# Optimization experiments

Hardware: AMD Instinct MI355X
Metric: run time of the kernel (lower is better)

Reference implementation:

```python
import math
import jax, jax.numpy as jnp
import numpy as np

D_MODEL = 1024
HEADS = 16
D_K = D_MODEL // HEADS
BATCH = 4
SEQ = 2048


def setup_inputs() -> dict:
    key = jax.random.key(0)
    ks = jax.random.split(key, 7)
    q = jax.random.normal(ks[0], (BATCH, SEQ, D_MODEL), dtype=jnp.float32)
    k = jax.random.normal(ks[1], (BATCH, SEQ, D_MODEL), dtype=jnp.float32)
    v = jax.random.normal(ks[2], (BATCH, SEQ, D_MODEL), dtype=jnp.float32)
    # causal mask: True = masked (filled with -inf), broadcastable over batch & heads
    mask = jnp.triu(jnp.ones((SEQ, SEQ), dtype=bool), k=1)[None, None, :, :]
    s = 1.0 / math.sqrt(D_MODEL)
    Wq = jax.random.normal(ks[3], (D_MODEL, D_MODEL), dtype=jnp.float32) * s
    Wk = jax.random.normal(ks[4], (D_MODEL, D_MODEL), dtype=jnp.float32) * s
    Wv = jax.random.normal(ks[5], (D_MODEL, D_MODEL), dtype=jnp.float32) * s
    Wo = jax.random.normal(ks[6], (D_MODEL, D_MODEL), dtype=jnp.float32) * s
    return {"q": q, "k": k, "v": v, "mask": mask, "Wq": Wq, "Wk": Wk, "Wv": Wv, "Wo": Wo}


def reference(q, k, v, mask, Wq, Wk, Wv, Wo):
    B, S, _ = q.shape
    # Linear(d_model, d_model, bias=False): y = x @ W.T
    def proj(x, W):
        return (x @ W.T).reshape(B, S, HEADS, D_K).transpose(0, 2, 1, 3)  # [B,H,S,Dk]
    qh, kh, vh = proj(q, Wq), proj(k, Wk), proj(v, Wv)
    scores = jnp.einsum('bhqd,bhkd->bhqk', qh, kh) / math.sqrt(D_K)
    scores = jnp.where(mask, -jnp.inf, scores)
    attn = jax.nn.softmax(scores, axis=-1)  # dropout p=0 is identity
    ctx = jnp.einsum('bhqk,bhkd->bhqd', attn, vh)
    ctx = ctx.transpose(0, 2, 1, 3).reshape(B, S, D_MODEL)
    return ctx @ Wo.T
```

## Files before the change

kernel.cpp:

```cpp
#include <hip/hip_runtime.h>
#include <hip/hip_bf16.h>
#include <stdint.h>

#define S_LEN 2048
#define DMODEL 1024
#define HEADS 16
#define DK 64
#define LDK 72

#define QSCALE 0.18033688011112042f

typedef __attribute__((ext_vector_type(8))) short bf16x8;
typedef __attribute__((ext_vector_type(4))) float f32x4;

__device__ __forceinline__ unsigned short f2bf(float f) {
    union { float f; unsigned u; } c; c.f = f;
    unsigned u = c.u;
    u += 0x7fffu + ((u >> 16) & 1u);
    return (unsigned short)(u >> 16);
}

__device__ __forceinline__ unsigned pkbf(float a, float b) {
    union { float f; unsigned u; } ca, cb; ca.f = a; cb.f = b;
    unsigned ua = ca.u + (0x7fffu + ((ca.u >> 16) & 1u));
    unsigned ub = cb.u + (0x7fffu + ((cb.u >> 16) & 1u));
    return __builtin_amdgcn_perm(ub, ua, 0x07060302);
}

__device__ __forceinline__ unsigned cvtpk(float a, float b) {
    unsigned r;
    asm("v_cvt_pk_bf16_f32 %0, %1, %2" : "=v"(r) : "v"(a), "v"(b));
    return r;
}

__device__ __forceinline__ void g2lds16(const unsigned short* g, unsigned short* l) {
    __builtin_amdgcn_global_load_lds((const __attribute__((address_space(1))) void*)g,
                                     (__attribute__((address_space(3))) void*)l, 16, 0, 0);
}

__global__ __launch_bounds__(256) void convert_kernel(
    const float* __restrict__ q, const float* __restrict__ k, const float* __restrict__ v,
    const float* __restrict__ Wq, const float* __restrict__ Wk, const float* __restrict__ Wv,
    const float* __restrict__ Wo,
    unsigned short* __restrict__ qbf, unsigned short* __restrict__ kbf,
    unsigned short* __restrict__ vbf, unsigned short* __restrict__ wbf)
{
    const float* src; unsigned short* dst; int n8;
    const int y = blockIdx.y;
    if (y == 0)      { src = q;  dst = qbf;           n8 = 1048576; }
    else if (y == 1) { src = k;  dst = kbf;           n8 = 1048576; }
    else if (y == 2) { src = v;  dst = vbf;           n8 = 1048576; }
    else if (y == 3) { src = Wq; dst = wbf;           n8 = 131072; }
    else if (y == 4) { src = Wk; dst = wbf + 1048576; n8 = 131072; }
    else if (y == 5) { src = Wv; dst = wbf + 2097152; n8 = 131072; }
    else             { src = Wo; dst = wbf + 3145728; n8 = 131072; }
    int i = blockIdx.x * 256 + threadIdx.x;
    if (i >= n8) return;
    float4 f0 = ((const float4*)src)[(size_t)2 * i];
    float4 f1 = ((const float4*)src)[(size_t)2 * i + 1];
    union { unsigned u[4]; uint4 v; } o;
    o.u[0] = pkbf(f0.x, f0.y); o.u[1] = pkbf(f0.z, f0.w);
    o.u[2] = pkbf(f1.x, f1.y); o.u[3] = pkbf(f1.z, f1.w);
    *(uint4*)&dst[(size_t)8 * i] = o.v;
}

__device__ __forceinline__ void gemm_core_256x128(
    const unsigned short* __restrict__ Apanel,
    const unsigned short* __restrict__ Bpanel,
    unsigned short* sm,
    f32x4 acc[4][4])
{
    const int t    = threadIdx.x;
    const int lane = t & 63;
    const int w    = t >> 6;
    const int wm   = w >> 1;
    const int wn   = w & 1;
    const int lrow = lane & 15;
    const int quad = lane >> 4;

    const int l8   = lane >> 3;
    const int c16s = (lane & 7) ^ l8;
    const unsigned short* gA = Apanel + (size_t)(w * 8 + l8) * 1024 + c16s * 8;
    const unsigned short* gB = Bpanel + (size_t)(w * 8 + l8) * 1024 + c16s * 8;
    unsigned short* lA = sm + w * 512;
    unsigned short* lB = sm + 16384 + w * 512;

#define STAGE_KT(bufsel, kt) do {                                         \
        unsigned short* la = lA + (bufsel) * 24576;                       \
        unsigned short* lb = lB + (bufsel) * 24576;                       \
        const unsigned short* ga = gA + (kt) * 64;                        \
        const unsigned short* gb = gB + (kt) * 64;                        \
        g2lds16(ga,                        la);                           \
        g2lds16(ga + (size_t) 64 * 1024,   la + 4096);                    \
        g2lds16(ga + (size_t)128 * 1024,   la + 8192);                    \
        g2lds16(ga + (size_t)192 * 1024,   la + 12288);                   \
        g2lds16(gb,                        lb);                           \
        g2lds16(gb + (size_t) 64 * 1024,   lb + 4096);                    \
    } while (0)

    for (int i = 0; i < 4; i++) for (int j = 0; j < 4; j++) acc[i][j] = (f32x4){0.f, 0.f, 0.f, 0.f};

    STAGE_KT(0, 0);

#pragma unroll 1
    for (int kt = 0; kt < 16; ++kt) {
        const int buf = kt & 1;
        if (kt < 15) {
            STAGE_KT(buf ^ 1, kt + 1);
            asm volatile("s_waitcnt vmcnt(6)" ::: "memory");
        } else {
            asm volatile("s_waitcnt vmcnt(0)" ::: "memory");
        }
        __builtin_amdgcn_sched_barrier(0);
        __builtin_amdgcn_s_barrier();
        __builtin_amdgcn_sched_barrier(0);

        const unsigned short* tA = sm + buf * 24576;
        const unsigned short* tB = sm + buf * 24576 + 16384;
        for (int kh = 0; kh < 2; ++kh) {
            const int cs = ((kh * 4 + quad) ^ (lrow & 7)) * 8;
            bf16x8 a[4], b[4];
            for (int mi = 0; mi < 4; mi++)
                a[mi] = *(const bf16x8*)&tA[(wm * 64 + mi * 16 + lrow) * 64 + cs];
            for (int nj = 0; nj < 4; nj++)
                b[nj] = *(const bf16x8*)&tB[(wn * 64 + nj * 16 + lrow) * 64 + cs];
            __builtin_amdgcn_s_setprio(1);
            for (int mi = 0; mi < 4; mi++)
                for (int nj = 0; nj < 4; nj++)
                    acc[mi][nj] = __builtin_amdgcn_mfma_f32_16x16x32_bf16(a[mi], b[nj], acc[mi][nj], 0, 0, 0);
            __builtin_amdgcn_s_setprio(0);
        }
        __builtin_amdgcn_sched_barrier(0);
        __builtin_amdgcn_s_barrier();
        __builtin_amdgcn_sched_barrier(0);
    }
#undef STAGE_KT
}

__global__ __launch_bounds__(512, 2) void proj_gemm_kernel(
    const unsigned short* __restrict__ qbf, const unsigned short* __restrict__ kbf,
    const unsigned short* __restrict__ vbf, const unsigned short* __restrict__ wbf,
    unsigned short* __restrict__ qh, unsigned short* __restrict__ kh,
    unsigned short* __restrict__ vh_t)
{
    const unsigned short* A; const unsigned short* Bm; unsigned short* Y;
    const int z = blockIdx.z;
    if (z == 0)      { A = qbf; Bm = wbf;           Y = qh;   }
    else if (z == 1) { A = kbf; Bm = wbf + 1048576; Y = kh;   }
    else             { A = vbf; Bm = wbf + 2097152; Y = vh_t; }

    __shared__ unsigned short sm[49152];

    const int m0 = blockIdx.x * 256;
    const int n0 = blockIdx.y * 128;

    f32x4 acc[4][4];
    gemm_core_256x128(A + (size_t)m0 * 1024, Bm + (size_t)n0 * 1024, sm, acc);

    const int t = threadIdx.x, lane = t & 63;
    const int wm = (t >> 6) >> 1, wn = (t >> 6) & 1;
    const int lrow = lane & 15, quad = lane >> 4;
    const float scale = (z == 0) ? QSCALE : 1.0f;
    for (int i = 0; i < 4; i++) {
        int grow = m0 + wm * 64 + i * 16 + quad * 4;
        for (int j = 0; j < 4; j++) {
            int gcol = n0 + wn * 64 + j * 16 + lrow;
            int h = gcol >> 6, d = gcol & 63;
            for (int r = 0; r < 4; r++) {
                int row = grow + r;
                int b_ = row >> 11;
                int s_ = row & 2047;
                unsigned short val = f2bf(acc[i][j][r] * scale);
                if (z == 2)
                    Y[(((size_t)(b_ * HEADS + h) * DK) + d) * S_LEN + s_] = val;
                else
                    Y[(((size_t)(b_ * HEADS + h) * S_LEN) + s_) * DK + d] = val;
            }
        }
    }
}

__global__ __launch_bounds__(512, 2) void outproj_gemm_kernel(
    const unsigned short* __restrict__ ctx, const unsigned short* __restrict__ wobf,
    float* __restrict__ out)
{
    __shared__ unsigned short sm[49152];

    const int m0 = blockIdx.x * 256;
    const int n0 = blockIdx.y * 128;

    f32x4 acc[4][4];
    gemm_core_256x128(ctx + (size_t)m0 * 1024, wobf + (size_t)n0 * 1024, sm, acc);

    const int t = threadIdx.x, lane = t & 63;
    const int wm = (t >> 6) >> 1, wn = (t >> 6) & 1;
    const int lrow = lane & 15, quad = lane >> 4;
    for (int i = 0; i < 4; i++) {
        int grow = m0 + wm * 64 + i * 16 + quad * 4;
        for (int j = 0; j < 4; j++) {
            int gcol = n0 + wn * 64 + j * 16 + lrow;
            for (int r = 0; r < 4; r++)
                out[(size_t)(grow + r) * DMODEL + gcol] = acc[i][j][r];
        }
    }
}

__global__ __launch_bounds__(256) void attn_kernel(
    const unsigned short* __restrict__ qh, const unsigned short* __restrict__ kh,
    const unsigned short* __restrict__ vh_t, unsigned short* __restrict__ ctx)
{
    __shared__ unsigned short sK[64 * LDK];
    __shared__ unsigned short sVt[64 * LDK];
    __shared__ unsigned short sPT[4][32 * LDK];

    const int t    = threadIdx.x;
    const int lane = t & 63;
    const int wid  = t >> 6;
    const int lin  = (int)(blockIdx.y * gridDim.x + blockIdx.x);
    const int wlin = (lin & 7) * 64 + (lin >> 3);
    const int qx   = wlin & 7;
    const int bh   = wlin >> 3;
    const size_t base = (size_t)bh * S_LEN * DK;
    const int lrow = lane & 15;
    const int quad = lane >> 4;
    const int b_ = bh >> 4, h_ = bh & 15;
    unsigned short* myPT = &sPT[wid][0];

    const int sr0 = t >> 3;
    const int sc0 = (t & 7) * 8;
    const unsigned short* gK = kh + base;
    const unsigned short* gV = vh_t + base;

    for (int pass = 0; pass < 2; ++pass) {
        const int qt = pass ? (15 - qx) : qx;
        const int q0 = qt * 128;
        const int qw0 = q0 + wid * 32;

        bf16x8 qreg[2][2];
        for (int nf = 0; nf < 2; ++nf)
            for (int h = 0; h < 2; ++h)
                qreg[nf][h] = *(const bf16x8*)&qh[base + (size_t)(qw0 + nf * 16 + lrow) * DK + h * 32 + quad * 8];

        f32x4 o[4][2];
        for (int mf = 0; mf < 4; mf++) for (int nf = 0; nf < 2; nf++) o[mf][nf] = (f32x4){0.f, 0.f, 0.f, 0.f};
        float lstat[2] = { 0.f, 0.f };

        const int ntiles = q0 / 64 + 2;

        uint4 rK0 = *(const uint4*)&gK[(size_t)sr0 * DK + sc0];
        uint4 rK1 = *(const uint4*)&gK[(size_t)(sr0 + 32) * DK + sc0];
        uint4 rV0 = *(const uint4*)&gV[(size_t)sr0 * S_LEN + sc0];
        uint4 rV1 = *(const uint4*)&gV[(size_t)(sr0 + 32) * S_LEN + sc0];

        for (int kt = 0; kt < ntiles; ++kt) {
            const int k0 = kt * 64;
            __syncthreads();
            *(uint4*)&sK [sr0 * LDK + sc0]        = rK0;
            *(uint4*)&sK [(sr0 + 32) * LDK + sc0] = rK1;
            *(uint4*)&sVt[sr0 * LDK + sc0]        = rV0;
            *(uint4*)&sVt[(sr0 + 32) * LDK + sc0] = rV1;
            if (kt + 1 < ntiles) {
                const int kn = k0 + 64;
                rK0 = *(const uint4*)&gK[(size_t)(kn + sr0) * DK + sc0];
                rK1 = *(const uint4*)&gK[(size_t)(kn + sr0 + 32) * DK + sc0];
                rV0 = *(const uint4*)&gV[(size_t)sr0 * S_LEN + kn + sc0];
                rV1 = *(const uint4*)&gV[(size_t)(sr0 + 32) * S_LEN + kn + sc0];
            }
            __syncthreads();

            if (k0 > qw0 + 31) continue;

            f32x4 st[4][2];
            for (int mf = 0; mf < 4; mf++) for (int nf = 0; nf < 2; nf++) st[mf][nf] = (f32x4){0.f, 0.f, 0.f, 0.f};
            for (int h = 0; h < 2; ++h) {
                bf16x8 kf[4];
                for (int mf = 0; mf < 4; mf++)
                    kf[mf] = *(const bf16x8*)&sK[(mf * 16 + lrow) * LDK + h * 32 + quad * 8];
                __builtin_amdgcn_s_setprio(1);
                for (int mf = 0; mf < 4; mf++)
                    for (int nf = 0; nf < 2; nf++)
                        st[mf][nf] = __builtin_amdgcn_mfma_f32_16x16x32_bf16(kf[mf], qreg[nf][h], st[mf][nf], 0, 0, 0);
                __builtin_amdgcn_s_setprio(0);
            }

            const bool need_mask = (k0 + 63 > qw0);

            for (int nf = 0; nf < 2; ++nf) {
                const int qidx = qw0 + nf * 16 + lrow;
                if (need_mask) {
                    for (int mf = 0; mf < 4; mf++)
                        for (int r = 0; r < 4; r++) {
                            int key = k0 + mf * 16 + quad * 4 + r;
                            if (key > qidx) st[mf][nf][r] = -INFINITY;
                        }
                }
                float rsum = 0.f;
                for (int mf = 0; mf < 4; mf++) {
                    float p0 = exp2f(st[mf][nf][0]);
                    float p1 = exp2f(st[mf][nf][1]);
                    float p2 = exp2f(st[mf][nf][2]);
                    float p3 = exp2f(st[mf][nf][3]);
                    rsum += (p0 + p1) + (p2 + p3);
                    uint2 pk;
                    pk.x = cvtpk(p0, p1);
                    pk.y = cvtpk(p2, p3);
                    *(uint2*)&myPT[(nf * 16 + lrow) * LDK + mf * 16 + quad * 4] = pk;
                }
                lstat[nf] += rsum;
            }

            for (int h = 0; h < 2; ++h) {
                bf16x8 vf[4], pf[2];
                for (int mf = 0; mf < 4; mf++)
                    vf[mf] = *(const bf16x8*)&sVt[(mf * 16 + lrow) * LDK + h * 32 + quad * 8];
                for (int nf = 0; nf < 2; nf++)
                    pf[nf] = *(const bf16x8*)&myPT[(nf * 16 + lrow) * LDK + h * 32 + quad * 8];
                __builtin_amdgcn_s_setprio(1);
                for (int mf = 0; mf < 4; mf++)
                    for (int nf = 0; nf < 2; nf++)
                        o[mf][nf] = __builtin_amdgcn_mfma_f32_16x16x32_bf16(vf[mf], pf[nf], o[mf][nf], 0, 0, 0);
                __builtin_amdgcn_s_setprio(0);
            }
        }

        for (int nf = 0; nf < 2; ++nf) {
            float ls = lstat[nf];
            ls += __shfl_xor(ls, 16);
            ls += __shfl_xor(ls, 32);
            float inv = 1.f / ls;
            int s_ = qw0 + nf * 16 + lrow;
            size_t rowbase = (((size_t)(b_ * S_LEN + s_)) * HEADS + h_) * DK;
            for (int mf = 0; mf < 4; mf++) {
                int d0 = mf * 16 + quad * 4;
                uint2 pk;
                pk.x = pkbf(o[mf][nf][0] * inv, o[mf][nf][1] * inv);
                pk.y = pkbf(o[mf][nf][2] * inv, o[mf][nf][3] * inv);
                *(uint2*)&ctx[rowbase + d0] = pk;
            }
        }
    }
}

__global__ __launch_bounds__(256) void proj_fb_kernel(
    const float* __restrict__ q, const float* __restrict__ k, const float* __restrict__ v,
    const float* __restrict__ Wq, const float* __restrict__ Wk, const float* __restrict__ Wv,
    unsigned short* __restrict__ qh, unsigned short* __restrict__ kh, unsigned short* __restrict__ vh_t)
{
    const float* X; const float* W; unsigned short* Y;
    if (blockIdx.z == 0)      { X = q; W = Wq; Y = qh; }
    else if (blockIdx.z == 1) { X = k; W = Wk; Y = kh; }
    else                      { X = v; W = Wv; Y = vh_t; }

    __shared__ short sA[128 * LDK];
    __shared__ short sB[128 * LDK];
    const int t = threadIdx.x, lane = t & 63, wid = t >> 6;
    const int wrow = (wid >> 1) * 64, wcol = (wid & 1) * 64;
    const int m0 = blockIdx.x * 128, n0 = blockIdx.y * 128;
    const int lrow = lane & 15, quad = lane >> 4, lk = quad * 8;

    f32x4 acc[4][4];
    for (int i = 0; i < 4; i++) for (int j = 0; j < 4; j++) acc[i][j] = (f32x4){0.f, 0.f, 0.f, 0.f};

    for (int kb = 0; kb < DMODEL; kb += 64) {
        for (int it = 0; it < 8; ++it) {
            int idx = t + it * 256;
            int row = idx >> 4, c4 = (idx & 15) * 4;
            float4 fa = *(const float4*)&X[(size_t)(m0 + row) * DMODEL + kb + c4];
            float4 fb = *(const float4*)&W[(size_t)(n0 + row) * DMODEL + kb + c4];
            short4 sa = { (short)f2bf(fa.x), (short)f2bf(fa.y), (short)f2bf(fa.z), (short)f2bf(fa.w) };
            short4 sb = { (short)f2bf(fb.x), (short)f2bf(fb.y), (short)f2bf(fb.z), (short)f2bf(fb.w) };
            *(short4*)&sA[row * LDK + c4] = sa;
            *(short4*)&sB[row * LDK + c4] = sb;
        }
        __syncthreads();
        for (int kk = 0; kk < 64; kk += 32) {
            bf16x8 a[4], b[4];
            for (int i = 0; i < 4; i++) a[i] = *(const bf16x8*)&sA[(wrow + i * 16 + lrow) * LDK + kk + lk];
            for (int j = 0; j < 4; j++) b[j] = *(const bf16x8*)&sB[(wcol + j * 16 + lrow) * LDK + kk + lk];
            for (int i = 0; i < 4; i++)
                for (int j = 0; j < 4; j++)
                    acc[i][j] = __builtin_amdgcn_mfma_f32_16x16x32_bf16(a[i], b[j], acc[i][j], 0, 0, 0);
        }
        __syncthreads();
    }

    const float scale = (blockIdx.z == 0) ? QSCALE : 1.0f;
    for (int i = 0; i < 4; i++) {
        int grow = m0 + wrow + i * 16 + quad * 4;
        for (int j = 0; j < 4; j++) {
            int gcol = n0 + wcol + j * 16 + lrow;
            int h = gcol >> 6, d = gcol & 63;
            for (int r = 0; r < 4; r++) {
                int row = grow + r, b_ = row >> 11, s_ = row & 2047;
                unsigned short val = f2bf(acc[i][j][r] * scale);
                if (blockIdx.z == 2)
                    Y[(((size_t)(b_ * HEADS + h) * DK) + d) * S_LEN + s_] = val;
                else
                    Y[(((size_t)(b_ * HEADS + h) * S_LEN) + s_) * DK + d] = val;
            }
        }
    }
}

__global__ __launch_bounds__(256) void outproj_fb_kernel(
    const unsigned short* __restrict__ ctx, const float* __restrict__ Wo, float* __restrict__ out)
{
    __shared__ short sA[128 * LDK];
    __shared__ short sB[128 * LDK];
    const int t = threadIdx.x, lane = t & 63, wid = t >> 6;
    const int wrow = (wid >> 1) * 64, wcol = (wid & 1) * 64;
    const int m0 = blockIdx.x * 128, n0 = blockIdx.y * 128;
    const int lrow = lane & 15, quad = lane >> 4, lk = quad * 8;

    f32x4 acc[4][4];
    for (int i = 0; i < 4; i++) for (int j = 0; j < 4; j++) acc[i][j] = (f32x4){0.f, 0.f, 0.f, 0.f};

    for (int kb = 0; kb < DMODEL; kb += 64) {
        for (int it = 0; it < 4; ++it) {
            int idx = t + it * 256;
            int row = idx >> 3, c8 = (idx & 7) * 8;
            *(uint4*)&sA[row * LDK + c8] = *(const uint4*)&ctx[(size_t)(m0 + row) * DMODEL + kb + c8];
        }
        for (int it = 0; it < 8; ++it) {
            int idx = t + it * 256;
            int row = idx >> 4, c4 = (idx & 15) * 4;
            float4 fb = *(const float4*)&Wo[(size_t)(n0 + row) * DMODEL + kb + c4];
            short4 sb = { (short)f2bf(fb.x), (short)f2bf(fb.y), (short)f2bf(fb.z), (short)f2bf(fb.w) };
            *(short4*)&sB[row * LDK + c4] = sb;
        }
        __syncthreads();
        for (int kk = 0; kk < 64; kk += 32) {
            bf16x8 a[4], b[4];
            for (int i = 0; i < 4; i++) a[i] = *(const bf16x8*)&sA[(wrow + i * 16 + lrow) * LDK + kk + lk];
            for (int j = 0; j < 4; j++) b[j] = *(const bf16x8*)&sB[(wcol + j * 16 + lrow) * LDK + kk + lk];
            for (int i = 0; i < 4; i++)
                for (int j = 0; j < 4; j++)
                    acc[i][j] = __builtin_amdgcn_mfma_f32_16x16x32_bf16(a[i], b[j], acc[i][j], 0, 0, 0);
        }
        __syncthreads();
    }

    for (int i = 0; i < 4; i++) {
        int grow = m0 + wrow + i * 16 + quad * 4;
        for (int j = 0; j < 4; j++) {
            int gcol = n0 + wcol + j * 16 + lrow;
            for (int r = 0; r < 4; r++)
                out[(size_t)(grow + r) * DMODEL + gcol] = acc[i][j][r];
        }
    }
}

extern "C" void kernel_launch(void* const* d_in, const int* in_sizes, int n_in,
                              void* d_out, int out_size, void* d_ws, size_t ws_size,
                              hipStream_t stream)
{
    const float* q  = (const float*)d_in[0];
    const float* k  = (const float*)d_in[1];
    const float* v  = (const float*)d_in[2];
    const float* Wq = (const float*)d_in[4];
    const float* Wk = (const float*)d_in[5];
    const float* Wv = (const float*)d_in[6];
    const float* Wo = (const float*)d_in[7];
    float* out = (float*)d_out;

    const size_t M8 = (size_t)8 * 1024 * 1024;
    const size_t need = (size_t)(52) * 1024 * 1024 * 2;

    if (ws_size >= need) {
        unsigned short* qbf  = (unsigned short*)d_ws;
        unsigned short* kbf  = qbf + M8;
        unsigned short* vbf  = kbf + M8;
        unsigned short* wbf  = vbf + M8;
        unsigned short* qh   = wbf + (size_t)4 * 1024 * 1024;
        unsigned short* kh   = qh + M8;
        unsigned short* vh_t = kh + M8;
        unsigned short* ctx  = qbf;

        dim3 gCvt(4096, 7);
        convert_kernel<<<gCvt, 256, 0, stream>>>(q, k, v, Wq, Wk, Wv, Wo, qbf, kbf, vbf, wbf);

        dim3 gProj(32, 8, 3);
        proj_gemm_kernel<<<gProj, 512, 0, stream>>>(qbf, kbf, vbf, wbf, qh, kh, vh_t);

        dim3 gAttn(8, 64);
        attn_kernel<<<gAttn, 256, 0, stream>>>(qh, kh, vh_t, ctx);

        dim3 gOut(32, 8);
        outproj_gemm_kernel<<<gOut, 512, 0, stream>>>(ctx, wbf + (size_t)3 * 1024 * 1024, out);
    } else {
        unsigned short* qh   = (unsigned short*)d_ws;
        unsigned short* kh   = qh + M8;
        unsigned short* vh_t = kh + M8;
        unsigned short* ctx  = vh_t + M8;

        dim3 gProj(64, 8, 3);
        proj_fb_kernel<<<gProj, 256, 0, stream>>>(q, k, v, Wq, Wk, Wv, qh, kh, vh_t);

        dim3 gAttn(8, 64);
        attn_kernel<<<gAttn, 256, 0, stream>>>(qh, kh, vh_t, ctx);

        dim3 gOut(64, 8);
        outproj_fb_kernel<<<gOut, 256, 0, stream>>>(ctx, Wo, out);
    }
}
```

Before: 326.8 us.

## Halve attention query tile to 64 rows and double block count

Attention blocks now handle a 64-row query tile per pass (16 rows per wave) instead of 128, with the grid doubled to 16x64 blocks and the causal mask applied only on the diagonal tile. Launch bounds request 4 blocks per CU and the per-wave P scratch is halved. This raises parallelism and occupancy and removes per-wave skipped tiles. In exchange, every K/V tile is loaded into shared memory twice as often per query row, and each wave issues fewer MFMAs per load.

```diff
diff --git a/kernel.cpp b/kernel.cpp
--- a/kernel.cpp
+++ b/kernel.cpp
@@ -205,21 +205,21 @@
     }
 }
 
-__global__ __launch_bounds__(256) void attn_kernel(
+__global__ __launch_bounds__(256, 4) void attn_kernel(
     const unsigned short* __restrict__ qh, const unsigned short* __restrict__ kh,
     const unsigned short* __restrict__ vh_t, unsigned short* __restrict__ ctx)
 {
     __shared__ unsigned short sK[64 * LDK];
     __shared__ unsigned short sVt[64 * LDK];
-    __shared__ unsigned short sPT[4][32 * LDK];
+    __shared__ unsigned short sPT[4][16 * LDK];
 
     const int t    = threadIdx.x;
     const int lane = t & 63;
     const int wid  = t >> 6;
     const int lin  = (int)(blockIdx.y * gridDim.x + blockIdx.x);
-    const int wlin = (lin & 7) * 64 + (lin >> 3);
-    const int qx   = wlin & 7;
-    const int bh   = wlin >> 3;
+    const int wlin = (lin & 7) * 128 + (lin >> 3);
+    const int qx   = wlin & 15;
+    const int bh   = wlin >> 4;
     const size_t base = (size_t)bh * S_LEN * DK;
     const int lrow = lane & 15;
     const int quad = lane >> 4;
@@ -232,20 +232,19 @@
     const unsigned short* gV = vh_t + base;
 
     for (int pass = 0; pass < 2; ++pass) {
-        const int qt = pass ? (15 - qx) : qx;
-        const int q0 = qt * 128;
-        const int qw0 = q0 + wid * 32;
-
-        bf16x8 qreg[2][2];
-        for (int nf = 0; nf < 2; ++nf)
-            for (int h = 0; h < 2; ++h)
-                qreg[nf][h] = *(const bf16x8*)&qh[base + (size_t)(qw0 + nf * 16 + lrow) * DK + h * 32 + quad * 8];
-
-        f32x4 o[4][2];
-        for (int mf = 0; mf < 4; mf++) for (int nf = 0; nf < 2; nf++) o[mf][nf] = (f32x4){0.f, 0.f, 0.f, 0.f};
-        float lstat[2] = { 0.f, 0.f };
-
-        const int ntiles = q0 / 64 + 2;
+        const int qt = pass ? (31 - qx) : qx;
+        const int q0 = qt * 64;
+        const int qw0 = q0 + wid * 16;
+
+        bf16x8 qreg[2];
+        for (int h = 0; h < 2; ++h)
+            qreg[h] = *(const bf16x8*)&qh[base + (size_t)(qw0 + lrow) * DK + h * 32 + quad * 8];
+
+        f32x4 o[4];
+        for (int mf = 0; mf < 4; mf++) o[mf] = (f32x4){0.f, 0.f, 0.f, 0.f};
+        float lstat = 0.f;
+
+        const int ntiles = qt + 1;
 
         uint4 rK0 = *(const uint4*)&gK[(size_t)sr0 * DK + sc0];
         uint4 rK1 = *(const uint4*)&gK[(size_t)(sr0 + 32) * DK + sc0];
@@ -268,73 +267,67 @@
             }
             __syncthreads();
 
-            if (k0 > qw0 + 31) continue;
-
-            f32x4 st[4][2];
-            for (int mf = 0; mf < 4; mf++) for (int nf = 0; nf < 2; nf++) st[mf][nf] = (f32x4){0.f, 0.f, 0.f, 0.f};
+            f32x4 st[4];
+            for (int mf = 0; mf < 4; mf++) st[mf] = (f32x4){0.f, 0.f, 0.f, 0.f};
             for (int h = 0; h < 2; ++h) {
                 bf16x8 kf[4];
                 for (int mf = 0; mf < 4; mf++)
                     kf[mf] = *(const bf16x8*)&sK[(mf * 16 + lrow) * LDK + h * 32 + quad * 8];
                 __builtin_amdgcn_s_setprio(1);
                 for (int mf = 0; mf < 4; mf++)
-                    for (int nf = 0; nf < 2; nf++)
-                        st[mf][nf] = __builtin_amdgcn_mfma_f32_16x16x32_bf16(kf[mf], qreg[nf][h], st[mf][nf], 0, 0, 0);
+                    st[mf] = __builtin_amdgcn_mfma_f32_16x16x32_bf16(kf[mf], qreg[h], st[mf], 0, 0, 0);
                 __builtin_amdgcn_s_setprio(0);
             }
 
-            const bool need_mask = (k0 + 63 > qw0);
-
-            for (int nf = 0; nf < 2; ++nf) {
-                const int qidx = qw0 + nf * 16 + lrow;
-                if (need_mask) {
-                    for (int mf = 0; mf < 4; mf++)
-                        for (int r = 0; r < 4; r++) {
-                            int key = k0 + mf * 16 + quad * 4 + r;
-                            if (key > qidx) st[mf][nf][r] = -INFINITY;
-                        }
-                }
+            if (kt == qt) {
+                const int qidx = qw0 + lrow;
+                for (int mf = 0; mf < 4; mf++)
+                    for (int r = 0; r < 4; r++) {
+                        int key = k0 + mf * 16 + quad * 4 + r;
+                        if (key > qidx) st[mf][r] = -INFINITY;
+                    }
+            }
+
+            {
                 float rsum = 0.f;
                 for (int mf = 0; mf < 4; mf++) {
-                    float p0 = exp2f(st[mf][nf][0]);
-                    float p1 = exp2f(st[mf][nf][1]);
-                    float p2 = exp2f(st[mf][nf][2]);
-                    float p3 = exp2f(st[mf][nf][3]);
+                    float p0 = exp2f(st[mf][0]);
+                    float p1 = exp2f(st[mf][1]);
+                    float p2 = exp2f(st[mf][2]);
+                    float p3 = exp2f(st[mf][3]);
                     rsum += (p0 + p1) + (p2 + p3);
                     uint2 pk;
                     pk.x = cvtpk(p0, p1);
                     pk.y = cvtpk(p2, p3);
-                    *(uint2*)&myPT[(nf * 16 + lrow) * LDK + mf * 16 + quad * 4] = pk;
+                    *(uint2*)&myPT[lrow * LDK + mf * 16 + quad * 4] = pk;
                 }
-                lstat[nf] += rsum;
+                lstat += rsum;
             }
 
             for (int h = 0; h < 2; ++h) {
-                bf16x8 vf[4], pf[2];
+                bf16x8 vf[4];
                 for (int mf = 0; mf < 4; mf++)
                     vf[mf] = *(const bf16x8*)&sVt[(mf * 16 + lrow) * LDK + h * 32 + quad * 8];
-                for (int nf = 0; nf < 2; nf++)
-                    pf[nf] = *(const bf16x8*)&myPT[(nf * 16 + lrow) * LDK + h * 32 + quad * 8];
+                bf16x8 pf = *(const bf16x8*)&myPT[lrow * LDK + h * 32 + quad * 8];
                 __builtin_amdgcn_s_setprio(1);
                 for (int mf = 0; mf < 4; mf++)
-                    for (int nf = 0; nf < 2; nf++)
-                        o[mf][nf] = __builtin_amdgcn_mfma_f32_16x16x32_bf16(vf[mf], pf[nf], o[mf][nf], 0, 0, 0);
+                    o[mf] = __builtin_amdgcn_mfma_f32_16x16x32_bf16(vf[mf], pf, o[mf], 0, 0, 0);
                 __builtin_amdgcn_s_setprio(0);
             }
         }
 
-        for (int nf = 0; nf < 2; ++nf) {
-            float ls = lstat[nf];
+        {
+            float ls = lstat;
             ls += __shfl_xor(ls, 16);
             ls += __shfl_xor(ls, 32);
             float inv = 1.f / ls;
-            int s_ = qw0 + nf * 16 + lrow;
+            int s_ = qw0 + lrow;
             size_t rowbase = (((size_t)(b_ * S_LEN + s_)) * HEADS + h_) * DK;
             for (int mf = 0; mf < 4; mf++) {
                 int d0 = mf * 16 + quad * 4;
                 uint2 pk;
-                pk.x = pkbf(o[mf][nf][0] * inv, o[mf][nf][1] * inv);
-                pk.y = pkbf(o[mf][nf][2] * inv, o[mf][nf][3] * inv);
+                pk.x = pkbf(o[mf][0] * inv, o[mf][1] * inv);
+                pk.y = pkbf(o[mf][2] * inv, o[mf][3] * inv);
                 *(uint2*)&ctx[rowbase + d0] = pk;
             }
         }
@@ -482,7 +475,7 @@
         dim3 gProj(32, 8, 3);
         proj_gemm_kernel<<<gProj, 512, 0, stream>>>(qbf, kbf, vbf, wbf, qh, kh, vh_t);
 
-        dim3 gAttn(8, 64);
+        dim3 gAttn(16, 64);
         attn_kernel<<<gAttn, 256, 0, stream>>>(qh, kh, vh_t, ctx);
 
         dim3 gOut(32, 8);
@@ -496,7 +489,7 @@
         dim3 gProj(64, 8, 3);
         proj_fb_kernel<<<gProj, 256, 0, stream>>>(q, k, v, Wq, Wk, Wv, qh, kh, vh_t);
 
-        dim3 gAttn(8, 64);
+        dim3 gAttn(16, 64);
         attn_kernel<<<gAttn, 256, 0, stream>>>(qh, kh, vh_t, ctx);
 
         dim3 gOut(64, 8);
```

Result: no change. 327.8 us (+0.3%).
